# Performance work log

Measured on AMD Instinct MI355X. Metric: run time of the kernel, lower is better.

Reference implementation:

```python
import jax, jax.numpy as jnp
import numpy as np
from jax import lax

FEAT_X, FEAT_Y = 50, 37          # generate_anchors(50, 37)
BASE_SIZE, DSR = 8.0, 16.0
A = FEAT_X * FEAT_Y * 9          # 16650 anchors


def generate_anchors():
    # Vectorized version of the triple python loop; order: x, y, size, [b1,b2,b3]
    xs = jnp.arange(FEAT_X, dtype=jnp.float32)[:, None, None]
    ys = jnp.arange(FEAT_Y, dtype=jnp.float32)[None, :, None]
    s = jnp.array([BASE_SIZE, 2 * BASE_SIZE, 4 * BASE_SIZE], jnp.float32)[None, None, :]

    def box(x1, y1, x2, y2):
        return jnp.stack(jnp.broadcast_arrays(x1 * DSR, y1 * DSR, x2 * DSR, y2 * DSR), axis=-1)

    b1 = box(xs - s / 2, ys - s / 2, xs + s / 2, ys + s / 2)      # square
    b2 = box(xs - s,     ys - s / 4, xs + s,     ys + s / 4)      # wide
    b3 = box(xs - s / 4, ys - s,     xs + s / 4, ys + s)          # tall
    anchors = jnp.stack([b1, b2, b3], axis=3)  # (50,37,3 sizes,3 variants,4)
    return anchors.reshape(-1, 4)              # (16650,4)


def conv2d(x, w, b, padding):
    y = lax.conv_general_dilated(x, w, (1, 1), padding,
                                 dimension_numbers=("NCHW", "OIHW", "NCHW"))
    return y + b[None, :, None, None]


def pairwise_iou(anchors, gt):
    # anchors: (A,4), gt: (B,G,4) -> iou (B,A,G); zero when no positive overlap
    a = anchors[None, :, None, :]
    g = gt[:, None, :, :]
    area_a = (a[..., 2] - a[..., 0]) * (a[..., 3] - a[..., 1])
    area_g = (g[..., 2] - g[..., 0]) * (g[..., 3] - g[..., 1])
    left = jnp.maximum(a[..., 0], g[..., 0])
    right = jnp.minimum(a[..., 2], g[..., 2])
    top = jnp.maximum(a[..., 1], g[..., 1])
    bot = jnp.minimum(a[..., 3], g[..., 3])
    no_ov = (left >= right) | (top >= bot)
    inter = jnp.where(no_ov, 0.0, (right - left) * (bot - top))
    return jnp.where(no_ov, 0.0, inter / (area_a + area_g - inter))


def setup_inputs() -> dict:
    key = jax.random.key(0)
    k1, k2, k3, k4, k5, k6, k7, k8 = jax.random.split(key, 8)
    B, G = 8, 20
    feats = jax.random.normal(k1, (B, 512, FEAT_Y, FEAT_X), jnp.float32)
    # well-formed gt boxes inside an ~800x592 image
    raw = jax.random.uniform(k2, (B, G, 2, 2)) * jnp.array([800.0, 592.0])
    x1y1 = jnp.min(raw, axis=2)
    x2y2 = jnp.max(raw, axis=2) + 1.0
    gt_boxes = jnp.concatenate([x1y1, x2y2], axis=-1)  # (B,G,4)
    im_info = jnp.array([[592.0, 800.0, 1.0]], jnp.float32)  # (h, w, scale)
    s = 0.02
    w3 = jax.random.normal(k3, (512, 512, 3, 3), jnp.float32) * s
    b3 = jnp.zeros((512,), jnp.float32)
    wc = jax.random.normal(k4, (18, 512, 1, 1), jnp.float32) * s
    bc = jnp.zeros((18,), jnp.float32)
    wb = jax.random.normal(k5, (36, 512, 1, 1), jnp.float32) * s
    bb = jnp.zeros((36,), jnp.float32)
    return {"feats": feats, "w3": w3, "b3": b3, "wc": wc, "bc": bc,
            "wb": wb, "bb": bb, "gt_boxes": gt_boxes, "im_info": im_info}


def reference(feats, w3, b3, wc, bc, wb, bb, gt_boxes, im_info):
    B = feats.shape[0]
    anchors = generate_anchors()
    rpn_conv1 = jax.nn.relu(conv2d(feats, w3, b3, ((1, 1), (1, 1))))
    rpn_cls_score = conv2d(rpn_conv1, wc, bc, ((0, 0), (0, 0)))  # (B,18,H,W)
    Bc, C, H, W = rpn_cls_score.shape
    score_rs = rpn_cls_score.reshape(Bc, 2, (C * H) // 2, W)      # reshape(x, 2)
    rpn_cls_prob = jax.nn.softmax(score_rs, axis=1).reshape(Bc, 18, H, W)
    rpn_bbox_pred = conv2d(rpn_conv1, wb, bb, ((0, 0), (0, 0)))   # (B,36,H,W)

    # anchor-target assignment (training branch), faithful to original logic
    inside = ((anchors[:, 0] >= 0) & (anchors[:, 1] >= 0) &
              (anchors[:, 2] < im_info[0, 1]) & (anchors[:, 3] < im_info[0, 0]))
    iou = pairwise_iou(anchors, gt_boxes)                 # (B,A,G)
    iou = jnp.where(inside[None, :, None], iou, 0.0)      # outside anchors skipped
    G = gt_boxes.shape[1]
    # original: idxs = argmax(iou_matrix[:][j]) with j == last gt index
    idx = jnp.argmax(iou[:, G - 1, :], axis=-1)           # (B,)
    labels = jnp.zeros((B, anchors.shape[0]), jnp.float32)
    labels = labels.at[jnp.arange(B), idx].set(1.0)
    max_iou = jnp.max(iou, axis=-1)                       # (B,A)
    labels = jnp.where(inside[None, :] & (max_iou > 0.7), 0.0, labels)

    out = jnp.concatenate([rpn_cls_prob, rpn_bbox_pred], axis=1)  # (B,54,H,W)
    return out, iou, labels
```

## Files before the change

### kernel.cpp

```cpp
#include <hip/hip_runtime.h>

typedef unsigned short u16;
typedef unsigned int u32;
typedef float f32x4 __attribute__((ext_vector_type(4)));
typedef short bf16x8 __attribute__((ext_vector_type(8)));

#define NB 8
#define FH 37
#define FW 50
#define FHW 1850
#define MTOT 14800
#define CIN 512
#define KTOT 4608
#define HP 39
#define WP 52
#define ANCH 16650
#define NG 20

#define ZB 356
#define WTB 9216
#define WHB 128
#define TRB 7424
#define IOB 528
#define PRE_TOT (ZB + WTB + WHB + TRB + IOB)

__device__ __forceinline__ u16 f2bf(float f) {
    u32 u = __float_as_uint(f);
    u += 0x7fffu + ((u >> 16) & 1u);
    return (u16)(u >> 16);
}

__device__ __forceinline__ void gl2lds16(const u16* g, u16* l) {
    __builtin_amdgcn_global_load_lds((const __attribute__((address_space(1))) void*)(g),
                                     (__attribute__((address_space(3))) void*)(l),
                                     16, 0, 0);
}

__device__ __forceinline__ void anchor_box(int a, float& x1, float& y1, float& x2, float& y2) {
    int x = a / 333;
    int rem = a - x * 333;
    int y = rem / 9;
    int r2 = rem - y * 9;
    int si = r2 / 3;
    int bi = r2 - si * 3;
    float s = (float)(8 << si);
    float fx = (float)x, fy = (float)y;
    float ax1, ay1, ax2, ay2;
    if (bi == 0)      { float h = s * 0.5f;  ax1 = fx - h; ay1 = fy - h; ax2 = fx + h; ay2 = fy + h; }
    else if (bi == 1) { float q = s * 0.25f; ax1 = fx - s; ay1 = fy - q; ax2 = fx + s; ay2 = fy + q; }
    else              { float q = s * 0.25f; ax1 = fx - q; ay1 = fy - s; ax2 = fx + q; ay2 = fy + s; }
    x1 = ax1 * 16.f; y1 = ay1 * 16.f; x2 = ax2 * 16.f; y2 = ay2 * 16.f;
}

__global__ __launch_bounds__(256) void k_pre(u16* __restrict__ apad,
                                             const float* __restrict__ w3, u16* __restrict__ wt,
                                             const float* __restrict__ wc, const float* __restrict__ wb,
                                             u16* __restrict__ whd,
                                             const float* __restrict__ feats,
                                             const float* __restrict__ gt, const float* __restrict__ im,
                                             float* __restrict__ iou_out, float* __restrict__ lab) {
    __shared__ __attribute__((aligned(16))) char smraw[20864];
    __shared__ int idxs;
    int blk = blockIdx.x;
    int t = threadIdx.x;

    if (blk < ZB) {
        uint4* apad4 = (uint4*)apad;
        int i = blk * 256 + t;
        int img = i / 11392;
        int r = i - img * 11392;
        int u4;
        if (r < 3328) u4 = r;
        else if (r < 6656) u4 = 126464 + (r - 3328);
        else {
            int rp = r - 6656;
            int h = 1 + (rp >> 7);
            int c2 = rp & 127;
            int col = (c2 & 64) ? 51 : 0;
            u4 = (h * 52 + col) * 64 + (c2 & 63);
        }
        apad4[img * 129792 + u4] = make_uint4(0u, 0u, 0u, 0u);
    } else if (blk < ZB + WTB) {
        int i = (blk - ZB) * 256 + t;
        int n = i / KTOT;
        int k = i - n * KTOT;
        int tap = k >> 9;
        int ci = k & 511;
        wt[i] = f2bf(w3[n * KTOT + ci * 9 + tap]);
    } else if (blk < ZB + WTB + WHB) {
        int i = (blk - ZB - WTB) * 256 + t;
        int n = i >> 9;
        int ci = i & 511;
        float v = 0.f;
        if (n < 18) v = wc[n * 512 + ci];
        else if (n < 54) v = wb[(n - 18) * 512 + ci];
        whd[i] = f2bf(v);
    } else if (blk < ZB + WTB + WHB + TRB) {
        float* tile = (float*)smraw;
        int q = blk - ZB - WTB - WHB;
        int xt = q % 58;
        int r2 = q / 58;
        int ct = r2 & 15;
        int img = r2 >> 4;
        int hw0 = xt * 32, c0 = ct * 32;
        int tx = t & 31, ty4 = t >> 5;
        #pragma unroll
        for (int rr = 0; rr < 4; rr++) {
            int ty = ty4 + rr * 8;
            int hw = hw0 + tx;
            if (hw < FHW) tile[ty * 33 + tx] = feats[(img * 512 + c0 + ty) * FHW + hw];
        }
        __syncthreads();
        #pragma unroll
        for (int rr = 0; rr < 4; rr++) {
            int ty = ty4 + rr * 8;
            int hw2 = hw0 + ty;
            if (hw2 < FHW) {
                int h = hw2 / FW, w = hw2 - h * FW;
                apad[(((img * HP) + h + 1) * WP + (w + 1)) * 512 + c0 + tx] = f2bf(tile[tx * 33 + ty]);
            }
        }
    } else {
        float* g4 = (float*)smraw;
        float* imv = g4 + 80;
        float* buf = g4 + 84;
        int q = blk - ZB - WTB - WHB - TRB;
        int at = q % 66;
        int b = q / 66;
        if (t < NG * 4) g4[t] = gt[b * NG * 4 + t];
        if (t < 2) imv[t] = im[t];
        __syncthreads();
        if (t == 0) {
            float x1, y1, x2, y2;
            anchor_box(19, x1, y1, x2, y2);
            bool inside = (x1 >= 0.f) && (y1 >= 0.f) && (x2 < imv[1]) && (y2 < imv[0]);
            float aa = (x2 - x1) * (y2 - y1);
            float best = -1.f; int bg = 0;
            for (int g = 0; g < NG; g++) {
                float gx1 = g4[g * 4], gy1 = g4[g * 4 + 1], gx2 = g4[g * 4 + 2], gy2 = g4[g * 4 + 3];
                float l = fmaxf(x1, gx1), r = fminf(x2, gx2);
                float tp = fmaxf(y1, gy1), bo = fminf(y2, gy2);
                float v = 0.f;
                if (l < r && tp < bo) {
                    float inter = (r - l) * (bo - tp);
                    float ag = (gx2 - gx1) * (gy2 - gy1);
                    v = inter / (aa + ag - inter);
                }
                if (!inside) v = 0.f;
                if (v > best) { best = v; bg = g; }
            }
            idxs = bg;
        }
        int a0 = at * 256;
        int a = a0 + t;
        float mx = 0.f;
        bool inside = false;
        if (a < ANCH) {
            float x1, y1, x2, y2;
            anchor_box(a, x1, y1, x2, y2);
            inside = (x1 >= 0.f) && (y1 >= 0.f) && (x2 < imv[1]) && (y2 < imv[0]);
            float aa = (x2 - x1) * (y2 - y1);
            for (int g = 0; g < NG; g++) {
                float gx1 = g4[g * 4], gy1 = g4[g * 4 + 1], gx2 = g4[g * 4 + 2], gy2 = g4[g * 4 + 3];
                float l = fmaxf(x1, gx1), r = fminf(x2, gx2);
                float tp = fmaxf(y1, gy1), bo = fminf(y2, gy2);
                float v = 0.f;
                if (l < r && tp < bo) {
                    float inter = (r - l) * (bo - tp);
                    float ag = (gx2 - gx1) * (gy2 - gy1);
                    v = inter / (aa + ag - inter);
                }
                if (!inside) v = 0.f;
                buf[t * NG + g] = v;
                mx = fmaxf(mx, v);
            }
        }
        __syncthreads();
        int rem = ANCH - a0;
        int cnt = (rem < 256 ? rem : 256) * NG;
        float* dst = iou_out + (b * ANCH + a0) * NG;
        for (int i = t; i < cnt; i += 256) dst[i] = buf[i];
        if (a < ANCH) {
            float lv = (a == idxs) ? 1.f : 0.f;
            if (inside && mx > 0.7f) lv = 0.f;
            lab[b * ANCH + a] = lv;
        }
    }
}

__global__ __launch_bounds__(256) void k_conv(const u16* __restrict__ apad,
                                              const u16* __restrict__ wt,
                                              const float* __restrict__ b3,
                                              u16* __restrict__ act) {
    __shared__ u16 As[128 * 64];
    __shared__ u16 Bs[64 * 64];
    int L = blockIdx.x;
    int mb = (L & 7) + 8 * (L >> 6);
    int nb = (L >> 3) & 7;
    if (mb >= 116) return;
    int tid = threadIdx.x;
    int wave = tid >> 6, lane = tid & 63;
    int m0 = mb * 128;
    int n0 = nb * 64;
    int wr = wave >> 1, wn = wave & 1;
    int lm = lane & 15, lq = lane >> 4;
    int l7 = lm & 7;

    f32x4 acc[4][2] = {};

    int rloc = tid >> 3;
    int cg = (tid & 7) ^ (rloc & 7);
    int aBase[4], bBase[2];
    for (int i = 0; i < 4; i++) {
        int m = m0 + i * 32 + rloc; if (m > MTOT - 1) m = MTOT - 1;
        int b = m / FHW; int hw = m - b * FHW;
        int h = hw / FW; int w = hw - h * FW;
        aBase[i] = ((b * HP + h) * WP + w) * 512 + cg * 8;
    }
    for (int j = 0; j < 2; j++)
        bBase[j] = (n0 + j * 32 + rloc) * KTOT + cg * 8;

    u16* aL[4]; u16* bL[2];
    for (int i = 0; i < 4; i++) aL[i] = &As[(i * 32 + wave * 8) * 64];
    for (int j = 0; j < 2; j++) bL[j] = &Bs[(j * 32 + wave * 8) * 64];

    for (int kk = 0; kk < KTOT; kk += 64) {
        int tap = kk >> 9;
        int ci0 = kk & 511;
        int dy = tap / 3, dx = tap - dy * 3;
        int aOfs = (dy * WP + dx) * 512 + ci0;
        gl2lds16(apad + aBase[0] + aOfs, aL[0]);
        gl2lds16(apad + aBase[1] + aOfs, aL[1]);
        gl2lds16(apad + aBase[2] + aOfs, aL[2]);
        gl2lds16(apad + aBase[3] + aOfs, aL[3]);
        gl2lds16(wt + bBase[0] + kk, bL[0]);
        gl2lds16(wt + bBase[1] + kk, bL[1]);
        __syncthreads();
        bf16x8 a[2][4], b[2][2];
        #pragma unroll
        for (int ks = 0; ks < 2; ks++) {
            int slotb = ((ks * 4 + lq) ^ l7) * 8;
            #pragma unroll
            for (int i = 0; i < 4; i++)
                a[ks][i] = *(const bf16x8*)&As[(wr * 64 + i * 16 + lm) * 64 + slotb];
            #pragma unroll
            for (int j = 0; j < 2; j++)
                b[ks][j] = *(const bf16x8*)&Bs[(wn * 32 + j * 16 + lm) * 64 + slotb];
        }
        #pragma unroll
        for (int ks = 0; ks < 2; ks++)
            #pragma unroll
            for (int i = 0; i < 4; i++)
                #pragma unroll
                for (int j = 0; j < 2; j++)
                    acc[i][j] = __builtin_amdgcn_mfma_f32_16x16x32_bf16(a[ks][i], b[ks][j], acc[i][j], 0, 0, 0);
        __syncthreads();
    }

    for (int j = 0; j < 2; j++) {
        int n = n0 + wn * 32 + j * 16 + lm;
        float bias = b3[n];
        for (int i = 0; i < 4; i++) {
            int mb2 = m0 + wr * 64 + i * 16 + lq * 4;
            for (int r = 0; r < 4; r++) {
                int m = mb2 + r;
                if (m < MTOT) {
                    float v = acc[i][j][r] + bias;
                    act[m * 512 + n] = f2bf(v > 0.f ? v : 0.f);
                }
            }
        }
    }
}

__global__ __launch_bounds__(256) void k_post(const u16* __restrict__ act,
                                              const u16* __restrict__ whd,
                                              const float* __restrict__ bc,
                                              const float* __restrict__ bb,
                                              float* __restrict__ out) {
    __shared__ float Sl[4 * 16 * 65];
    int tid = threadIdx.x;
    int wave = tid >> 6, lane = tid & 63;
    int lm = lane & 15, lq = lane >> 4;
    int m0 = blockIdx.x * 64 + wave * 16;
    int mr = m0 + lm; if (mr > MTOT - 1) mr = MTOT - 1;
    const u16* arow = act + mr * 512;
    f32x4 acc[4] = {};
    for (int kk = 0; kk < 512; kk += 32) {
        bf16x8 a = *(const bf16x8*)&arow[kk + lq * 8];
        #pragma unroll
        for (int j = 0; j < 4; j++) {
            bf16x8 b = *(const bf16x8*)&whd[(j * 16 + lm) * 512 + kk + lq * 8];
            acc[j] = __builtin_amdgcn_mfma_f32_16x16x32_bf16(a, b, acc[j], 0, 0, 0);
        }
    }
    float* S = &Sl[wave * 1040];
    #pragma unroll
    for (int r = 0; r < 4; r++)
        #pragma unroll
        for (int j = 0; j < 4; j++)
            S[(lq * 4 + r) * 65 + j * 16 + lm] = acc[j][r];
    __syncthreads();
    int r16 = lane & 15, cg = lane >> 4;
    int m = m0 + r16;
    if (m < MTOT) {
        int b = m / FHW, hw = m - b * FHW;
        const float* Sr = &S[r16 * 65];
        #pragma unroll
        for (int k = 0; k < 14; k++) {
            int c = cg + 4 * k;
            if (c >= 54) break;
            float v;
            if (c < 18) {
                int c0 = c < 9 ? c : c - 9;
                float s0 = Sr[c0] + bc[c0];
                float s1 = Sr[c0 + 9] + bc[c0 + 9];
                float mx = fmaxf(s0, s1);
                float e0 = __expf(s0 - mx), e1 = __expf(s1 - mx);
                v = (c < 9 ? e0 : e1) / (e0 + e1);
            } else {
                v = Sr[c] + bb[c - 18];
            }
            out[(b * 54 + c) * FHW + hw] = v;
        }
    }
}

extern "C" void kernel_launch(void* const* d_in, const int* in_sizes, int n_in,
                              void* d_out, int out_size, void* d_ws, size_t ws_size,
                              hipStream_t stream) {
    (void)in_sizes; (void)n_in; (void)out_size; (void)ws_size;
    const float* feats = (const float*)d_in[0];
    const float* w3    = (const float*)d_in[1];
    const float* b3    = (const float*)d_in[2];
    const float* wc    = (const float*)d_in[3];
    const float* bc    = (const float*)d_in[4];
    const float* wb    = (const float*)d_in[5];
    const float* bb    = (const float*)d_in[6];
    const float* gt    = (const float*)d_in[7];
    const float* im    = (const float*)d_in[8];
    float* out = (float*)d_out;
    char* ws = (char*)d_ws;

    u16* apad = (u16*)(ws);
    u16* wt   = (u16*)(ws + 16613376);
    u16* whd  = (u16*)(ws + 21331968);
    u16* act  = (u16*)(ws + 21397504);

    float* iou_out = out + 799200;
    float* lab     = out + 3463200;

    k_pre<<<dim3(PRE_TOT), dim3(256), 0, stream>>>(apad, w3, wt, wc, wb, whd,
                                                   feats, gt, im, iou_out, lab);
    k_conv<<<dim3(960), dim3(256), 0, stream>>>(apad, wt, b3, act);
    k_post<<<dim3(232), dim3(256), 0, stream>>>(act, whd, bc, bb, out);
}
```

Before: 210.3 us.

## Split conv K across two blocks, fuse reduction into head GEMM, move IoU into conv launch

The 3x3 conv GEMM now splits the K dimension in half, so twice as many blocks (1856) each write fp32 partial sums to a workspace buffer. The head kernel sums the two partials, adds bias, applies ReLU and converts to bf16 in LDS before its own MFMA GEMM, which is also split over K across waves. The IoU/label work moves from the pre-kernel into the conv launch so it overlaps with the GEMM, and the weight transpose now stages each row through LDS for coalesced reads. In exchange it adds fp32 partial-sum traffic of roughly 2x14800x512x4 bytes written and read back.

```diff
diff --git a/kernel.cpp b/kernel.cpp
--- a/kernel.cpp
+++ b/kernel.cpp
@@ -16,13 +16,17 @@
 #define WP 52
 #define ANCH 16650
 #define NG 20
+#define MPAD 14848
+#define PSTRIDE 7602176
 
 #define ZB 356
-#define WTB 9216
+#define WTB 512
 #define WHB 128
 #define TRB 7424
+#define PRE_TOT (ZB + WTB + WHB + TRB)
+
+#define CONVB 1856
 #define IOB 528
-#define PRE_TOT (ZB + WTB + WHB + TRB + IOB)
 
 __device__ __forceinline__ u16 f2bf(float f) {
     u32 u = __float_as_uint(f);
@@ -56,11 +60,8 @@
                                              const float* __restrict__ w3, u16* __restrict__ wt,
                                              const float* __restrict__ wc, const float* __restrict__ wb,
                                              u16* __restrict__ whd,
-                                             const float* __restrict__ feats,
-                                             const float* __restrict__ gt, const float* __restrict__ im,
-                                             float* __restrict__ iou_out, float* __restrict__ lab) {
-    __shared__ __attribute__((aligned(16))) char smraw[20864];
-    __shared__ int idxs;
+                                             const float* __restrict__ feats) {
+    __shared__ __attribute__((aligned(16))) char smraw[18432];
     int blk = blockIdx.x;
     int t = threadIdx.x;
 
@@ -81,12 +82,16 @@
         }
         apad4[img * 129792 + u4] = make_uint4(0u, 0u, 0u, 0u);
     } else if (blk < ZB + WTB) {
-        int i = (blk - ZB) * 256 + t;
-        int n = i / KTOT;
-        int k = i - n * KTOT;
-        int tap = k >> 9;
-        int ci = k & 511;
-        wt[i] = f2bf(w3[n * KTOT + ci * 9 + tap]);
+        float* lt = (float*)smraw;
+        int n = blk - ZB;
+        const float* src = w3 + n * KTOT;
+        for (int i = t; i < KTOT; i += 256) lt[i] = src[i];
+        __syncthreads();
+        u16* dst = wt + n * KTOT;
+        for (int o = t; o < KTOT; o += 256) {
+            int tap = o >> 9, ci = o & 511;
+            dst[o] = f2bf(lt[ci * 9 + tap]);
+        }
     } else if (blk < ZB + WTB + WHB) {
         int i = (blk - ZB - WTB) * 256 + t;
         int n = i >> 9;
@@ -95,7 +100,7 @@
         if (n < 18) v = wc[n * 512 + ci];
         else if (n < 54) v = wb[(n - 18) * 512 + ci];
         whd[i] = f2bf(v);
-    } else if (blk < ZB + WTB + WHB + TRB) {
+    } else {
         float* tile = (float*)smraw;
         int q = blk - ZB - WTB - WHB;
         int xt = q % 58;
@@ -120,13 +125,107 @@
                 apad[(((img * HP) + h + 1) * WP + (w + 1)) * 512 + c0 + tx] = f2bf(tile[tx * 33 + ty]);
             }
         }
+    }
+}
+
+__global__ __launch_bounds__(256) void k_conv(const u16* __restrict__ apad,
+                                              const u16* __restrict__ wt,
+                                              float* __restrict__ P,
+                                              const float* __restrict__ gt,
+                                              const float* __restrict__ im,
+                                              float* __restrict__ iou_out,
+                                              float* __restrict__ lab) {
+    __shared__ __attribute__((aligned(16))) char sm[24576];
+    __shared__ int idxs;
+    int L = blockIdx.x;
+    int tid = threadIdx.x;
+
+    if (L < CONVB) {
+        u16* As = (u16*)sm;
+        u16* Bs = (u16*)(sm + 16384);
+        int g = L >> 6;
+        int pair = (L & 7) + 8 * g;
+        int nb = (L >> 3) & 7;
+        int mb = pair >> 1;
+        int kh = pair & 1;
+        int wave = tid >> 6, lane = tid & 63;
+        int m0 = mb * 128;
+        int n0 = nb * 64;
+        int wr = wave >> 1, wn = wave & 1;
+        int lm = lane & 15, lq = lane >> 4;
+        int l7 = lm & 7;
+
+        f32x4 acc[4][2] = {};
+
+        int rloc = tid >> 3;
+        int cg = (tid & 7) ^ (rloc & 7);
+        int aBase[4], bBase[2];
+        for (int i = 0; i < 4; i++) {
+            int m = m0 + i * 32 + rloc; if (m > MTOT - 1) m = MTOT - 1;
+            int b = m / FHW; int hw = m - b * FHW;
+            int h = hw / FW; int w = hw - h * FW;
+            aBase[i] = ((b * HP + h) * WP + w) * 512 + cg * 8;
+        }
+        for (int j = 0; j < 2; j++)
+            bBase[j] = (n0 + j * 32 + rloc) * KTOT + cg * 8;
+
+        u16* aL[4]; u16* bL[2];
+        for (int i = 0; i < 4; i++) aL[i] = &As[(i * 32 + wave * 8) * 64];
+        for (int j = 0; j < 2; j++) bL[j] = &Bs[(j * 32 + wave * 8) * 64];
+
+        int kEnd = (kh + 1) * 2304;
+        for (int kk = kh * 2304; kk < kEnd; kk += 64) {
+            int tap = kk >> 9;
+            int ci0 = kk & 511;
+            int dy = tap / 3, dx = tap - dy * 3;
+            int aOfs = (dy * WP + dx) * 512 + ci0;
+            gl2lds16(apad + aBase[0] + aOfs, aL[0]);
+            gl2lds16(apad + aBase[1] + aOfs, aL[1]);
+            gl2lds16(apad + aBase[2] + aOfs, aL[2]);
+            gl2lds16(apad + aBase[3] + aOfs, aL[3]);
+            gl2lds16(wt + bBase[0] + kk, bL[0]);
+            gl2lds16(wt + bBase[1] + kk, bL[1]);
+            __syncthreads();
+            bf16x8 a[2][4], b[2][2];
+            #pragma unroll
+            for (int ks = 0; ks < 2; ks++) {
+                int slotb = ((ks * 4 + lq) ^ l7) * 8;
+                #pragma unroll
+                for (int i = 0; i < 4; i++)
+                    a[ks][i] = *(const bf16x8*)&As[(wr * 64 + i * 16 + lm) * 64 + slotb];
+                #pragma unroll
+                for (int j = 0; j < 2; j++)
+                    b[ks][j] = *(const bf16x8*)&Bs[(wn * 32 + j * 16 + lm) * 64 + slotb];
+            }
+            #pragma unroll
+            for (int ks = 0; ks < 2; ks++)
+                #pragma unroll
+                for (int i = 0; i < 4; i++)
+                    #pragma unroll
+                    for (int j = 0; j < 2; j++)
+                        acc[i][j] = __builtin_amdgcn_mfma_f32_16x16x32_bf16(a[ks][i], b[ks][j], acc[i][j], 0, 0, 0);
+            __syncthreads();
+        }
+
+        float* Pp = P + (size_t)kh * PSTRIDE;
+        for (int j = 0; j < 2; j++) {
+            int n = n0 + wn * 32 + j * 16 + lm;
+            for (int i = 0; i < 4; i++) {
+                int mb2 = m0 + wr * 64 + i * 16 + lq * 4;
+                for (int r = 0; r < 4; r++) {
+                    int m = mb2 + r;
+                    if (m < MTOT) Pp[m * 512 + n] = acc[i][j][r];
+                }
+            }
+        }
     } else {
-        float* g4 = (float*)smraw;
+        float* g4 = (float*)sm;
         float* imv = g4 + 80;
         float* buf = g4 + 84;
-        int q = blk - ZB - WTB - WHB - TRB;
+        int q = L - CONVB;
         int at = q % 66;
         int b = q / 66;
+        int t = tid;
         if (t < NG * 4) g4[t] = gt[b * NG * 4 + t];
         if (t < 2) imv[t] = im[t];
         __syncthreads();
@@ -136,8 +235,8 @@
             bool inside = (x1 >= 0.f) && (y1 >= 0.f) && (x2 < imv[1]) && (y2 < imv[0]);
             float aa = (x2 - x1) * (y2 - y1);
             float best = -1.f; int bg = 0;
-            for (int g = 0; g < NG; g++) {
-                float gx1 = g4[g * 4], gy1 = g4[g * 4 + 1], gx2 = g4[g * 4 + 2], gy2 = g4[g * 4 + 3];
+            for (int g2 = 0; g2 < NG; g2++) {
+                float gx1 = g4[g2 * 4], gy1 = g4[g2 * 4 + 1], gx2 = g4[g2 * 4 + 2], gy2 = g4[g2 * 4 + 3];
                 float l = fmaxf(x1, gx1), r = fminf(x2, gx2);
                 float tp = fmaxf(y1, gy1), bo = fminf(y2, gy2);
                 float v = 0.f;
@@ -147,7 +246,7 @@
                     v = inter / (aa + ag - inter);
                 }
                 if (!inside) v = 0.f;
-                if (v > best) { best = v; bg = g; }
+                if (v > best) { best = v; bg = g2; }
             }
             idxs = bg;
         }
@@ -160,8 +259,8 @@
             anchor_box(a, x1, y1, x2, y2);
             inside = (x1 >= 0.f) && (y1 >= 0.f) && (x2 < imv[1]) && (y2 < imv[0]);
             float aa = (x2 - x1) * (y2 - y1);
-            for (int g = 0; g < NG; g++) {
-                float gx1 = g4[g * 4], gy1 = g4[g * 4 + 1], gx2 = g4[g * 4 + 2], gy2 = g4[g * 4 + 3];
+            for (int g2 = 0; g2 < NG; g2++) {
+                float gx1 = g4[g2 * 4], gy1 = g4[g2 * 4 + 1], gx2 = g4[g2 * 4 + 2], gy2 = g4[g2 * 4 + 3];
                 float l = fmaxf(x1, gx1), r = fminf(x2, gx2);
                 float tp = fmaxf(y1, gy1), bo = fminf(y2, gy2);
                 float v = 0.f;
@@ -171,7 +270,7 @@
                     v = inter / (aa + ag - inter);
                 }
                 if (!inside) v = 0.f;
-                buf[t * NG + g] = v;
+                buf[t * NG + g2] = v;
                 mx = fmaxf(mx, v);
             }
         }
@@ -188,141 +287,81 @@
     }
 }
 
-__global__ __launch_bounds__(256) void k_conv(const u16* __restrict__ apad,
-                                              const u16* __restrict__ wt,
+__global__ __launch_bounds__(256) void k_post(const float* __restrict__ P,
+                                              const u16* __restrict__ whd,
                                               const float* __restrict__ b3,
-                                              u16* __restrict__ act) {
-    __shared__ u16 As[128 * 64];
-    __shared__ u16 Bs[64 * 64];
-    int L = blockIdx.x;
-    int mb = (L & 7) + 8 * (L >> 6);
-    int nb = (L >> 3) & 7;
-    if (mb >= 116) return;
-    int tid = threadIdx.x;
-    int wave = tid >> 6, lane = tid & 63;
-    int m0 = mb * 128;
-    int n0 = nb * 64;
-    int wr = wave >> 1, wn = wave & 1;
-    int lm = lane & 15, lq = lane >> 4;
-    int l7 = lm & 7;
-
-    f32x4 acc[4][2] = {};
-
-    int rloc = tid >> 3;
-    int cg = (tid & 7) ^ (rloc & 7);
-    int aBase[4], bBase[2];
-    for (int i = 0; i < 4; i++) {
-        int m = m0 + i * 32 + rloc; if (m > MTOT - 1) m = MTOT - 1;
-        int b = m / FHW; int hw = m - b * FHW;
-        int h = hw / FW; int w = hw - h * FW;
-        aBase[i] = ((b * HP + h) * WP + w) * 512 + cg * 8;
-    }
-    for (int j = 0; j < 2; j++)
-        bBase[j] = (n0 + j * 32 + rloc) * KTOT + cg * 8;
-
-    u16* aL[4]; u16* bL[2];
-    for (int i = 0; i < 4; i++) aL[i] = &As[(i * 32 + wave * 8) * 64];
-    for (int j = 0; j < 2; j++) bL[j] = &Bs[(j * 32 + wave * 8) * 64];
-
-    for (int kk = 0; kk < KTOT; kk += 64) {
-        int tap = kk >> 9;
-        int ci0 = kk & 511;
-        int dy = tap / 3, dx = tap - dy * 3;
-        int aOfs = (dy * WP + dx) * 512 + ci0;
-        gl2lds16(apad + aBase[0] + aOfs, aL[0]);
-        gl2lds16(apad + aBase[1] + aOfs, aL[1]);
-        gl2lds16(apad + aBase[2] + aOfs, aL[2]);
-        gl2lds16(apad + aBase[3] + aOfs, aL[3]);
-        gl2lds16(wt + bBase[0] + kk, bL[0]);
-        gl2lds16(wt + bBase[1] + kk, bL[1]);
-        __syncthreads();
-        bf16x8 a[2][4], b[2][2];
-        #pragma unroll
-        for (int ks = 0; ks < 2; ks++) {
-            int slotb = ((ks * 4 + lq) ^ l7) * 8;
-            #pragma unroll
-            for (int i = 0; i < 4; i++)
-                a[ks][i] = *(const bf16x8*)&As[(wr * 64 + i * 16 + lm) * 64 + slotb];
-            #pragma unroll
-            for (int j = 0; j < 2; j++)
-                b[ks][j] = *(const bf16x8*)&Bs[(wn * 32 + j * 16 + lm) * 64 + slotb];
-        }
-        #pragma unroll
-        for (int ks = 0; ks < 2; ks++)
-            #pragma unroll
-            for (int i = 0; i < 4; i++)
-                #pragma unroll
-                for (int j = 0; j < 2; j++)
-                    acc[i][j] = __builtin_amdgcn_mfma_f32_16x16x32_bf16(a[ks][i], b[ks][j], acc[i][j], 0, 0, 0);
-        __syncthreads();
-    }
-
-    for (int j = 0; j < 2; j++) {
-        int n = n0 + wn * 32 + j * 16 + lm;
-        float bias = b3[n];
-        for (int i = 0; i < 4; i++) {
-            int mb2 = m0 + wr * 64 + i * 16 + lq * 4;
-            for (int r = 0; r < 4; r++) {
-                int m = mb2 + r;
-                if (m < MTOT) {
-                    float v = acc[i][j][r] + bias;
-                    act[m * 512 + n] = f2bf(v > 0.f ? v : 0.f);
-                }
-            }
-        }
-    }
-}
-
-__global__ __launch_bounds__(256) void k_post(const u16* __restrict__ act,
-                                              const u16* __restrict__ whd,
                                               const float* __restrict__ bc,
                                               const float* __restrict__ bb,
                                               float* __restrict__ out) {
-    __shared__ float Sl[4 * 16 * 65];
-    int tid = threadIdx.x;
-    int wave = tid >> 6, lane = tid & 63;
-    int lm = lane & 15, lq = lane >> 4;
-    int m0 = blockIdx.x * 64 + wave * 16;
-    int mr = m0 + lm; if (mr > MTOT - 1) mr = MTOT - 1;
-    const u16* arow = act + mr * 512;
+    __shared__ __attribute__((aligned(16))) u16 actT[32 * 64 * 8];
+    __shared__ float Sl[4][16][68];
+    int t = threadIdx.x;
+    int m0 = blockIdx.x * 32;
+    const float* P0 = P;
+    const float* P1 = P + PSTRIDE;
+
+    #pragma unroll
+    for (int i = 0; i < 16; i++) {
+        int idx = t + i * 256;
+        int row = idx >> 7, col4 = idx & 127;
+        size_t off = (size_t)(m0 + row) * 512 + col4 * 4;
+        f32x4 p0 = *(const f32x4*)&P0[off];
+        f32x4 p1 = *(const f32x4*)&P1[off];
+        f32x4 bi = *(const f32x4*)&b3[col4 * 4];
+        u32 lo, hi;
+        {
+            float v0 = p0[0] + p1[0] + bi[0]; v0 = v0 > 0.f ? v0 : 0.f;
+            float v1 = p0[1] + p1[1] + bi[1]; v1 = v1 > 0.f ? v1 : 0.f;
+            float v2 = p0[2] + p1[2] + bi[2]; v2 = v2 > 0.f ? v2 : 0.f;
+            float v3 = p0[3] + p1[3] + bi[3]; v3 = v3 > 0.f ? v3 : 0.f;
+            lo = (u32)f2bf(v0) | ((u32)f2bf(v1) << 16);
+            hi = (u32)f2bf(v2) | ((u32)f2bf(v3) << 16);
+        }
+        int slot = row * 64 + ((col4 >> 1) ^ (row & 7));
+        *(uint2*)&actT[slot * 8 + (col4 & 1) * 4] = make_uint2(lo, hi);
+    }
+    __syncthreads();
+
+    int wave = t >> 6, lane = t & 63, lm = lane & 15, lq = lane >> 4;
+    int g = wave >> 1, kh = wave & 1;
+    int rowLoc = g * 16 + lm;
     f32x4 acc[4] = {};
-    for (int kk = 0; kk < 512; kk += 32) {
-        bf16x8 a = *(const bf16x8*)&arow[kk + lq * 8];
+    #pragma unroll
+    for (int s = 0; s < 8; s++) {
+        int kk = kh * 256 + s * 32;
+        int c = (kk >> 3) + lq;
+        bf16x8 a = *(const bf16x8*)&actT[(rowLoc * 64 + (c ^ (rowLoc & 7))) * 8];
         #pragma unroll
         for (int j = 0; j < 4; j++) {
             bf16x8 b = *(const bf16x8*)&whd[(j * 16 + lm) * 512 + kk + lq * 8];
             acc[j] = __builtin_amdgcn_mfma_f32_16x16x32_bf16(a, b, acc[j], 0, 0, 0);
         }
     }
-    float* S = &Sl[wave * 1040];
     #pragma unroll
     for (int r = 0; r < 4; r++)
         #pragma unroll
         for (int j = 0; j < 4; j++)
-            S[(lq * 4 + r) * 65 + j * 16 + lm] = acc[j][r];
+            Sl[wave][lq * 4 + r][j * 16 + lm] = acc[j][r];
     __syncthreads();
-    int r16 = lane & 15, cg = lane >> 4;
-    int m = m0 + r16;
-    if (m < MTOT) {
+
+    for (int i = t; i < 32 * 54; i += 256) {
+        int row = i & 31, cc = i >> 5;
+        int m = m0 + row;
+        if (m >= MTOT) continue;
+        int g2 = (row >> 4) * 2, rl = row & 15;
+        float v;
+        if (cc < 18) {
+            int c0 = cc < 9 ? cc : cc - 9;
+            float s0 = Sl[g2][rl][c0] + Sl[g2 + 1][rl][c0] + bc[c0];
+            float s1 = Sl[g2][rl][c0 + 9] + Sl[g2 + 1][rl][c0 + 9] + bc[c0 + 9];
+            float mx = fmaxf(s0, s1);
+            float e0 = __expf(s0 - mx), e1 = __expf(s1 - mx);
+            v = (cc < 9 ? e0 : e1) / (e0 + e1);
+        } else {
+            v = Sl[g2][rl][cc] + Sl[g2 + 1][rl][cc] + bb[cc - 18];
+        }
         int b = m / FHW, hw = m - b * FHW;
-        const float* Sr = &S[r16 * 65];
-        #pragma unroll
-        for (int k = 0; k < 14; k++) {
-            int c = cg + 4 * k;
-            if (c >= 54) break;
-            float v;
-            if (c < 18) {
-                int c0 = c < 9 ? c : c - 9;
-                float s0 = Sr[c0] + bc[c0];
-                float s1 = Sr[c0 + 9] + bc[c0 + 9];
-                float mx = fmaxf(s0, s1);
-                float e0 = __expf(s0 - mx), e1 = __expf(s1 - mx);
-                v = (c < 9 ? e0 : e1) / (e0 + e1);
-            } else {
-                v = Sr[c] + bb[c - 18];
-            }
-            out[(b * 54 + c) * FHW + hw] = v;
-        }
+        out[(b * 54 + cc) * FHW + hw] = v;
     }
 }
 
@@ -345,13 +384,12 @@
     u16* apad = (u16*)(ws);
     u16* wt   = (u16*)(ws + 16613376);
     u16* whd  = (u16*)(ws + 21331968);
-    u16* act  = (u16*)(ws + 21397504);
+    float* P  = (float*)(ws + 21397504);
 
     float* iou_out = out + 799200;
     float* lab     = out + 3463200;
 
-    k_pre<<<dim3(PRE_TOT), dim3(256), 0, stream>>>(apad, w3, wt, wc, wb, whd,
-                                                   feats, gt, im, iou_out, lab);
-    k_conv<<<dim3(960), dim3(256), 0, stream>>>(apad, wt, b3, act);
-    k_post<<<dim3(232), dim3(256), 0, stream>>>(act, whd, bc, bb, out);
-}
+    k_pre<<<dim3(PRE_TOT), dim3(256), 0, stream>>>(apad, w3, wt, wc, wb, whd, feats);
+    k_conv<<<dim3(CONVB + IOB), dim3(256), 0, stream>>>(apad, wt, P, gt, im, iou_out, lab);
+    k_post<<<dim3(464), dim3(256), 0, stream>>>(P, whd, b3, bc, bb, out);
+}
```

Measured after the change: 206.8 us. About the same (-1.7%).

## Coalesce weight transpose via LDS, widen feature transpose, move IoU into conv kernel

Applied to the files above, without the earlier changes.

The 3x3 weight reorder now runs one block per output channel, staging the row in LDS so global reads are contiguous instead of strided by 9. The feature transpose handles 64 channels per block and writes packed bf16 pairs as 32-bit stores. The IoU/label blocks move from the preprocessing kernel into the conv launch as extra blocks, so that independent work overlaps the GEMM tail. The cost is a larger LDS footprint in the conv kernel, which may lower occupancy, and a mixed-role grid.

```diff
diff --git a/kernel.cpp b/kernel.cpp
--- a/kernel.cpp
+++ b/kernel.cpp
@@ -18,11 +18,13 @@
 #define NG 20
 
 #define ZB 356
-#define WTB 9216
+#define WTB 512
 #define WHB 128
-#define TRB 7424
+#define TRB 3712
+#define PRE_TOT (ZB + WTB + WHB + TRB)
+
+#define CONVB 960
 #define IOB 528
-#define PRE_TOT (ZB + WTB + WHB + TRB + IOB)
 
 __device__ __forceinline__ u16 f2bf(float f) {
     u32 u = __float_as_uint(f);
@@ -56,11 +58,8 @@
                                              const float* __restrict__ w3, u16* __restrict__ wt,
                                              const float* __restrict__ wc, const float* __restrict__ wb,
                                              u16* __restrict__ whd,
-                                             const float* __restrict__ feats,
-                                             const float* __restrict__ gt, const float* __restrict__ im,
-                                             float* __restrict__ iou_out, float* __restrict__ lab) {
-    __shared__ __attribute__((aligned(16))) char smraw[20864];
-    __shared__ int idxs;
+                                             const float* __restrict__ feats) {
+    __shared__ __attribute__((aligned(16))) char smraw[18432];
     int blk = blockIdx.x;
     int t = threadIdx.x;
 
@@ -81,12 +80,16 @@
         }
         apad4[img * 129792 + u4] = make_uint4(0u, 0u, 0u, 0u);
     } else if (blk < ZB + WTB) {
-        int i = (blk - ZB) * 256 + t;
-        int n = i / KTOT;
-        int k = i - n * KTOT;
-        int tap = k >> 9;
-        int ci = k & 511;
-        wt[i] = f2bf(w3[n * KTOT + ci * 9 + tap]);
+        float* lt = (float*)smraw;
+        int n = blk - ZB;
+        const float* src = w3 + n * KTOT;
+        for (int i = t; i < KTOT; i += 256) lt[i] = src[i];
+        __syncthreads();
+        u16* dst = wt + n * KTOT;
+        for (int o = t; o < KTOT; o += 256) {
+            int tap = o >> 9, ci = o & 511;
+            dst[o] = f2bf(lt[ci * 9 + tap]);
+        }
     } else if (blk < ZB + WTB + WHB) {
         int i = (blk - ZB - WTB) * 256 + t;
         int n = i >> 9;
@@ -95,38 +98,137 @@
         if (n < 18) v = wc[n * 512 + ci];
         else if (n < 54) v = wb[(n - 18) * 512 + ci];
         whd[i] = f2bf(v);
-    } else if (blk < ZB + WTB + WHB + TRB) {
+    } else {
         float* tile = (float*)smraw;
         int q = blk - ZB - WTB - WHB;
         int xt = q % 58;
         int r2 = q / 58;
-        int ct = r2 & 15;
-        int img = r2 >> 4;
-        int hw0 = xt * 32, c0 = ct * 32;
-        int tx = t & 31, ty4 = t >> 5;
+        int ct = r2 & 7;
+        int img = r2 >> 3;
+        int hw0 = xt * 32, c0 = ct * 64;
+        int lx = t & 31, ly = t >> 5;
+        #pragma unroll
+        for (int rr = 0; rr < 8; rr++) {
+            int cl = ly + rr * 8;
+            int hw = hw0 + lx;
+            if (hw < FHW) tile[cl * 33 + lx] = feats[(img * 512 + c0 + cl) * FHW + hw];
+        }
+        __syncthreads();
         #pragma unroll
         for (int rr = 0; rr < 4; rr++) {
-            int ty = ty4 + rr * 8;
-            int hw = hw0 + tx;
-            if (hw < FHW) tile[ty * 33 + tx] = feats[(img * 512 + c0 + ty) * FHW + hw];
-        }
-        __syncthreads();
-        #pragma unroll
-        for (int rr = 0; rr < 4; rr++) {
-            int ty = ty4 + rr * 8;
-            int hw2 = hw0 + ty;
+            int hwl = ly + rr * 8;
+            int hw2 = hw0 + hwl;
             if (hw2 < FHW) {
                 int h = hw2 / FW, w = hw2 - h * FW;
-                apad[(((img * HP) + h + 1) * WP + (w + 1)) * 512 + c0 + tx] = f2bf(tile[tx * 33 + ty]);
+                float v0 = tile[(2 * lx) * 33 + hwl];
+                float v1 = tile[(2 * lx + 1) * 33 + hwl];
+                u32 pk = (u32)f2bf(v0) | ((u32)f2bf(v1) << 16);
+                u32* dst = (u32*)&apad[(((img * HP) + h + 1) * WP + (w + 1)) * 512 + c0];
+                dst[lx] = pk;
+            }
+        }
+    }
+}
+
+__global__ __launch_bounds__(256) void k_conv(const u16* __restrict__ apad,
+                                              const u16* __restrict__ wt,
+                                              const float* __restrict__ b3,
+                                              u16* __restrict__ act,
+                                              const float* __restrict__ gt,
+                                              const float* __restrict__ im,
+                                              float* __restrict__ iou_out,
+                                              float* __restrict__ lab) {
+    __shared__ __attribute__((aligned(16))) char sm[24576];
+    __shared__ int idxs;
+    int L = blockIdx.x;
+    int tid = threadIdx.x;
+
+    if (L < CONVB) {
+        u16* As = (u16*)sm;
+        u16* Bs = (u16*)(sm + 16384);
+        int mb = (L & 7) + 8 * (L >> 6);
+        int nb = (L >> 3) & 7;
+        if (mb >= 116) return;
+        int wave = tid >> 6, lane = tid & 63;
+        int m0 = mb * 128;
+        int n0 = nb * 64;
+        int wr = wave >> 1, wn = wave & 1;
+        int lm = lane & 15, lq = lane >> 4;
+        int l7 = lm & 7;
+
+        f32x4 acc[4][2] = {};
+
+        int rloc = tid >> 3;
+        int cg = (tid & 7) ^ (rloc & 7);
+        int aBase[4], bBase[2];
+        for (int i = 0; i < 4; i++) {
+            int m = m0 + i * 32 + rloc; if (m > MTOT - 1) m = MTOT - 1;
+            int b = m / FHW; int hw = m - b * FHW;
+            int h = hw / FW; int w = hw - h * FW;
+            aBase[i] = ((b * HP + h) * WP + w) * 512 + cg * 8;
+        }
+        for (int j = 0; j < 2; j++)
+            bBase[j] = (n0 + j * 32 + rloc) * KTOT + cg * 8;
+
+        u16* aL[4]; u16* bL[2];
+        for (int i = 0; i < 4; i++) aL[i] = &As[(i * 32 + wave * 8) * 64];
+        for (int j = 0; j < 2; j++) bL[j] = &Bs[(j * 32 + wave * 8) * 64];
+
+        for (int kk = 0; kk < KTOT; kk += 64) {
+            int tap = kk >> 9;
+            int ci0 = kk & 511;
+            int dy = tap / 3, dx = tap - dy * 3;
+            int aOfs = (dy * WP + dx) * 512 + ci0;
+            gl2lds16(apad + aBase[0] + aOfs, aL[0]);
+            gl2lds16(apad + aBase[1] + aOfs, aL[1]);
+            gl2lds16(apad + aBase[2] + aOfs, aL[2]);
+            gl2lds16(apad + aBase[3] + aOfs, aL[3]);
+            gl2lds16(wt + bBase[0] + kk, bL[0]);
+            gl2lds16(wt + bBase[1] + kk, bL[1]);
+            __syncthreads();
+            bf16x8 a[2][4], b[2][2];
+            #pragma unroll
+            for (int ks = 0; ks < 2; ks++) {
+                int slotb = ((ks * 4 + lq) ^ l7) * 8;
+                #pragma unroll
+                for (int i = 0; i < 4; i++)
+                    a[ks][i] = *(const bf16x8*)&As[(wr * 64 + i * 16 + lm) * 64 + slotb];
+                #pragma unroll
+                for (int j = 0; j < 2; j++)
+                    b[ks][j] = *(const bf16x8*)&Bs[(wn * 32 + j * 16 + lm) * 64 + slotb];
+            }
+            #pragma unroll
+            for (int ks = 0; ks < 2; ks++)
+                #pragma unroll
+                for (int i = 0; i < 4; i++)
+                    #pragma unroll
+                    for (int j = 0; j < 2; j++)
+                        acc[i][j] = __builtin_amdgcn_mfma_f32_16x16x32_bf16(a[ks][i], b[ks][j], acc[i][j], 0, 0, 0);
+            __syncthreads();
+        }
+
+        for (int j = 0; j < 2; j++) {
+            int n = n0 + wn * 32 + j * 16 + lm;
+            float bias = b3[n];
+            for (int i = 0; i < 4; i++) {
+                int mb2 = m0 + wr * 64 + i * 16 + lq * 4;
+                for (int r = 0; r < 4; r++) {
+                    int m = mb2 + r;
+                    if (m < MTOT) {
+                        float v = acc[i][j][r] + bias;
+                        act[m * 512 + n] = f2bf(v > 0.f ? v : 0.f);
+                    }
+                }
             }
         }
     } else {
-        float* g4 = (float*)smraw;
+        float* g4 = (float*)sm;
         float* imv = g4 + 80;
         float* buf = g4 + 84;
-        int q = blk - ZB - WTB - WHB - TRB;
+        int q = L - CONVB;
         int at = q % 66;
         int b = q / 66;
+        int t = tid;
         if (t < NG * 4) g4[t] = gt[b * NG * 4 + t];
         if (t < 2) imv[t] = im[t];
         __syncthreads();
@@ -136,8 +238,8 @@
             bool inside = (x1 >= 0.f) && (y1 >= 0.f) && (x2 < imv[1]) && (y2 < imv[0]);
             float aa = (x2 - x1) * (y2 - y1);
             float best = -1.f; int bg = 0;
-            for (int g = 0; g < NG; g++) {
-                float gx1 = g4[g * 4], gy1 = g4[g * 4 + 1], gx2 = g4[g * 4 + 2], gy2 = g4[g * 4 + 3];
+            for (int g2 = 0; g2 < NG; g2++) {
+                float gx1 = g4[g2 * 4], gy1 = g4[g2 * 4 + 1], gx2 = g4[g2 * 4 + 2], gy2 = g4[g2 * 4 + 3];
                 float l = fmaxf(x1, gx1), r = fminf(x2, gx2);
                 float tp = fmaxf(y1, gy1), bo = fminf(y2, gy2);
                 float v = 0.f;
@@ -147,7 +249,7 @@
                     v = inter / (aa + ag - inter);
                 }
                 if (!inside) v = 0.f;
-                if (v > best) { best = v; bg = g; }
+                if (v > best) { best = v; bg = g2; }
             }
             idxs = bg;
         }
@@ -160,8 +262,8 @@
             anchor_box(a, x1, y1, x2, y2);
             inside = (x1 >= 0.f) && (y1 >= 0.f) && (x2 < imv[1]) && (y2 < imv[0]);
             float aa = (x2 - x1) * (y2 - y1);
-            for (int g = 0; g < NG; g++) {
-                float gx1 = g4[g * 4], gy1 = g4[g * 4 + 1], gx2 = g4[g * 4 + 2], gy2 = g4[g * 4 + 3];
+            for (int g2 = 0; g2 < NG; g2++) {
+                float gx1 = g4[g2 * 4], gy1 = g4[g2 * 4 + 1], gx2 = g4[g2 * 4 + 2], gy2 = g4[g2 * 4 + 3];
                 float l = fmaxf(x1, gx1), r = fminf(x2, gx2);
                 float tp = fmaxf(y1, gy1), bo = fminf(y2, gy2);
                 float v = 0.f;
@@ -171,104 +273,19 @@
                     v = inter / (aa + ag - inter);
                 }
                 if (!inside) v = 0.f;
-                buf[t * NG + g] = v;
+                buf[t * NG + g2] = v;
                 mx = fmaxf(mx, v);
             }
         }
         __syncthreads();
         int rem = ANCH - a0;
-        int cnt = (rem < 256 ? rem : 256) * NG;
+        int cnt2 = (rem < 256 ? rem : 256) * NG;
         float* dst = iou_out + (b * ANCH + a0) * NG;
-        for (int i = t; i < cnt; i += 256) dst[i] = buf[i];
+        for (int i = t; i < cnt2; i += 256) dst[i] = buf[i];
         if (a < ANCH) {
             float lv = (a == idxs) ? 1.f : 0.f;
             if (inside && mx > 0.7f) lv = 0.f;
             lab[b * ANCH + a] = lv;
-        }
-    }
-}
-
-__global__ __launch_bounds__(256) void k_conv(const u16* __restrict__ apad,
-                                              const u16* __restrict__ wt,
-                                              const float* __restrict__ b3,
-                                              u16* __restrict__ act) {
-    __shared__ u16 As[128 * 64];
-    __shared__ u16 Bs[64 * 64];
-    int L = blockIdx.x;
-    int mb = (L & 7) + 8 * (L >> 6);
-    int nb = (L >> 3) & 7;
-    if (mb >= 116) return;
-    int tid = threadIdx.x;
-    int wave = tid >> 6, lane = tid & 63;
-    int m0 = mb * 128;
-    int n0 = nb * 64;
-    int wr = wave >> 1, wn = wave & 1;
-    int lm = lane & 15, lq = lane >> 4;
-    int l7 = lm & 7;
-
-    f32x4 acc[4][2] = {};
-
-    int rloc = tid >> 3;
-    int cg = (tid & 7) ^ (rloc & 7);
-    int aBase[4], bBase[2];
-    for (int i = 0; i < 4; i++) {
-        int m = m0 + i * 32 + rloc; if (m > MTOT - 1) m = MTOT - 1;
-        int b = m / FHW; int hw = m - b * FHW;
-        int h = hw / FW; int w = hw - h * FW;
-        aBase[i] = ((b * HP + h) * WP + w) * 512 + cg * 8;
-    }
-    for (int j = 0; j < 2; j++)
-        bBase[j] = (n0 + j * 32 + rloc) * KTOT + cg * 8;
-
-    u16* aL[4]; u16* bL[2];
-    for (int i = 0; i < 4; i++) aL[i] = &As[(i * 32 + wave * 8) * 64];
-    for (int j = 0; j < 2; j++) bL[j] = &Bs[(j * 32 + wave * 8) * 64];
-
-    for (int kk = 0; kk < KTOT; kk += 64) {
-        int tap = kk >> 9;
-        int ci0 = kk & 511;
-        int dy = tap / 3, dx = tap - dy * 3;
-        int aOfs = (dy * WP + dx) * 512 + ci0;
-        gl2lds16(apad + aBase[0] + aOfs, aL[0]);
-        gl2lds16(apad + aBase[1] + aOfs, aL[1]);
-        gl2lds16(apad + aBase[2] + aOfs, aL[2]);
-        gl2lds16(apad + aBase[3] + aOfs, aL[3]);
-        gl2lds16(wt + bBase[0] + kk, bL[0]);
-        gl2lds16(wt + bBase[1] + kk, bL[1]);
-        __syncthreads();
-        bf16x8 a[2][4], b[2][2];
-        #pragma unroll
-        for (int ks = 0; ks < 2; ks++) {
-            int slotb = ((ks * 4 + lq) ^ l7) * 8;
-            #pragma unroll
-            for (int i = 0; i < 4; i++)
-                a[ks][i] = *(const bf16x8*)&As[(wr * 64 + i * 16 + lm) * 64 + slotb];
-            #pragma unroll
-            for (int j = 0; j < 2; j++)
-                b[ks][j] = *(const bf16x8*)&Bs[(wn * 32 + j * 16 + lm) * 64 + slotb];
-        }
-        #pragma unroll
-        for (int ks = 0; ks < 2; ks++)
-            #pragma unroll
-            for (int i = 0; i < 4; i++)
-                #pragma unroll
-                for (int j = 0; j < 2; j++)
-                    acc[i][j] = __builtin_amdgcn_mfma_f32_16x16x32_bf16(a[ks][i], b[ks][j], acc[i][j], 0, 0, 0);
-        __syncthreads();
-    }
-
-    for (int j = 0; j < 2; j++) {
-        int n = n0 + wn * 32 + j * 16 + lm;
-        float bias = b3[n];
-        for (int i = 0; i < 4; i++) {
-            int mb2 = m0 + wr * 64 + i * 16 + lq * 4;
-            for (int r = 0; r < 4; r++) {
-                int m = mb2 + r;
-                if (m < MTOT) {
-                    float v = acc[i][j][r] + bias;
-                    act[m * 512 + n] = f2bf(v > 0.f ? v : 0.f);
-                }
-            }
         }
     }
 }
@@ -350,8 +367,7 @@
     float* iou_out = out + 799200;
     float* lab     = out + 3463200;
 
-    k_pre<<<dim3(PRE_TOT), dim3(256), 0, stream>>>(apad, w3, wt, wc, wb, whd,
-                                                   feats, gt, im, iou_out, lab);
-    k_conv<<<dim3(960), dim3(256), 0, stream>>>(apad, wt, b3, act);
+    k_pre<<<dim3(PRE_TOT), dim3(256), 0, stream>>>(apad, w3, wt, wc, wb, whd, feats);
+    k_conv<<<dim3(CONVB + IOB), dim3(256), 0, stream>>>(apad, wt, b3, act, gt, im, iou_out, lab);
     k_post<<<dim3(232), dim3(256), 0, stream>>>(act, whd, bc, bb, out);
 }
```

Measured after the change: 200.4 us (median of 2 runs). 4.7% less time.
